# Performance work log

Hardware: AMD Instinct MI355X
Metric: run time of the kernel (lower is better)

## Reference

```python
import jax, jax.numpy as jnp
import numpy as np

B = 256        # batch of LLR frames
N = 576        # code length (from wman_N0576_R34_z24)
MR = 144       # check rows = N * (1 - 3/4)
Z = 24         # lifting factor
IT = 3         # decoding iterations
ROW_DEG = 15   # check-node degree (WiMAX rate-3/4)


def setup_inputs() -> dict:
    key = jax.random.key(0)
    r = jax.random.normal(key, (B, N), dtype=jnp.float32)
    # Deterministic sparse Tanner graph: 15 ones per check row (>=2 required for top-2)
    rng = np.random.RandomState(0)
    Hnp = np.zeros((MR, N), dtype=np.int32)
    cols = np.argsort(rng.rand(MR, N), axis=1)[:, :ROW_DEG]
    Hnp[np.arange(MR)[:, None], cols] = 1
    H = jnp.asarray(Hnp)
    alpha = jnp.ones((MR // Z, N // Z, IT), dtype=jnp.float32) * 0.7
    beta = jnp.ones((MR // Z, N // Z, IT), dtype=jnp.float32) * 0.05
    return {"r": r, "alpha": alpha, "beta": beta, "H": H}


def _decode(r, alpha, beta, Hf):
    # r: (B, N) channel LLRs; Hf: (MR, N) float 0/1 parity-check mask
    mask = Hf == 1.0
    node = jnp.arange(N)[None, None, :]           # (1, 1, N)
    M = Hf[None, :, :] * r[:, None, :]            # initial v->c messages (B, MR, N)
    E = jnp.zeros_like(M)
    n_it = alpha.shape[-1]
    for it in range(n_it):
        a = jnp.repeat(jnp.repeat(alpha[:, :, it], Z, axis=0), Z, axis=1)  # (MR, N)
        bt = jnp.repeat(jnp.repeat(beta[:, :, it], Z, axis=0), Z, axis=1)  # (MR, N)
        # check -> variable: masked min-2 magnitude + extrinsic sign product
        abs_M = jnp.abs(M)
        masked = jnp.where(mask, abs_M, jnp.inf)
        neg_vals, idx = jax.lax.top_k(-masked, 2)  # two smallest per check row
        min_vals = -neg_vals                        # (B, MR, 2)
        # exclude self: use 2nd min at the argmin position, 1st min elsewhere
        E_abs = jnp.where(node == idx[..., 0:1], min_vals[..., 1:2], min_vals[..., 0:1])
        signs = jnp.where(mask, jnp.sign(M), 1.0)
        row_sign_prod = jnp.prod(signs, axis=2, keepdims=True)
        E_sign = row_sign_prod * signs              # extrinsic sign
        E = a * E_sign * jax.nn.relu(E_abs - bt) * Hf
        # variable -> check: sum-minus-self
        sum_E = jnp.sum(E, axis=1, keepdims=True)   # (B, 1, N)
        M = (r[:, None, :] + sum_E - E) * Hf
    return r + jnp.sum(E, axis=1)                   # posterior LLRs (B, N)


def reference(r, alpha, beta, H):
    return _decode(r, alpha, beta, H.astype(jnp.float32))
```

## Files before the change

### kernel.cpp

```cpp
#include <hip/hip_runtime.h>

#define BATCH   256
#define NCOL    576
#define MROW    144
#define ZLIFT   24
#define NIT     3
#define ROW_DEG 15
#define NEDGE   (MROW * ROW_DEG)
#define NSCIT   ((MROW/ZLIFT) * (NCOL/ZLIFT) * NIT)
#define TPB     512

__global__ __launch_bounds__(256) void build_cols_kernel(
    const int* __restrict__ H, int* __restrict__ pk)
{
    const int wave = (blockIdx.x * blockDim.x + threadIdx.x) >> 6;
    const int lane = threadIdx.x & 63;
    if (wave >= MROW) return;
    const int* row = H + (size_t)wave * NCOL;
    const int srow = (wave / ZLIFT) * (NCOL / ZLIFT);
    int base = 0;
    #pragma unroll
    for (int c0 = 0; c0 < NCOL; c0 += 64) {
        const int n = c0 + lane;
        const int present = (row[n] != 0) ? 1 : 0;
        const unsigned long long mask = __ballot(present);
        if (present) {
            const int rank = __popcll(mask & ((1ull << lane) - 1ull));
            const int idx = base + rank;
            if (idx < ROW_DEG)
                pk[wave * ROW_DEG + idx] = n | ((srow + n / ZLIFT) << 16);
        }
        base += __popcll(mask);
    }
}

__global__ __launch_bounds__(TPB) void ldpc_decode_kernel(
    const float* __restrict__ r,
    const float* __restrict__ alpha,
    const float* __restrict__ beta,
    const int*   __restrict__ pk,
    float*       __restrict__ out)
{
    __shared__ float r_s[NCOL];
    __shared__ float cs[2][NCOL];
    __shared__ float E_s[NEDGE];
    __shared__ float a_s[NSCIT];
    __shared__ float b_s[NSCIT];
    __shared__ int   cdeg[NCOL];
    __shared__ int   cstart[NCOL];

    const int b   = blockIdx.x;
    const int tid = threadIdx.x;

    for (int n = tid; n < NCOL; n += TPB) {
        r_s[n]   = r[(size_t)b * NCOL + n];
        cs[0][n] = 0.0f;
        cdeg[n]  = 0;
    }
    if (tid < NSCIT) { a_s[tid] = alpha[tid]; b_s[tid] = beta[tid]; }
    __syncthreads();

    const bool is_row = (tid < MROW);
    int   pk_r[ROW_DEG];
    float r_r[ROW_DEG];
    float E_r[ROW_DEG];
    int   slot_r[ROW_DEG];
    if (is_row) {
        #pragma unroll
        for (int k = 0; k < ROW_DEG; ++k) {
            const int p = pk[tid * ROW_DEG + k];
            pk_r[k] = p;
            const int n = p & 0xFFFF;
            r_r[k]  = r_s[n];
            E_r[k]  = 0.0f;
            slot_r[k] = atomicAdd(&cdeg[n], 1);
        }
    }
    __syncthreads();

    if (tid < 64) {
        int local[9];
        int run = 0;
        #pragma unroll
        for (int j = 0; j < 9; ++j) { local[j] = cdeg[tid * 9 + j]; run += local[j]; }
        int scan = run;
        #pragma unroll
        for (int off = 1; off < 64; off <<= 1) {
            int up = __shfl_up(scan, off);
            if (tid >= off) scan += up;
        }
        int acc = scan - run;
        #pragma unroll
        for (int j = 0; j < 9; ++j) { cstart[tid * 9 + j] = acc; acc += local[j]; }
    }
    __syncthreads();

    if (is_row) {
        #pragma unroll
        for (int k = 0; k < ROW_DEG; ++k)
            slot_r[k] += cstart[pk_r[k] & 0xFFFF];
    }

    for (int it = 0; it < NIT; ++it) {
        float* prev = cs[it & 1];
        float* next = cs[(it + 1) & 1];

        if (is_row) {
            float vals[ROW_DEG];
            float min1 = INFINITY, min2 = INFINITY;
            int   kmin = -1;
            float sprod = 1.0f;
            #pragma unroll
            for (int k = 0; k < ROW_DEG; ++k) {
                const int n = pk_r[k] & 0xFFFF;
                const float v = r_r[k] + prev[n] - E_r[k];
                vals[k] = v;
                const float av = fabsf(v);
                const float s = (v > 0.0f) ? 1.0f : ((v < 0.0f) ? -1.0f : 0.0f);
                sprod *= s;
                if (av < min1)      { min2 = min1; min1 = av; kmin = k; }
                else if (av < min2) { min2 = av; }
            }
            #pragma unroll
            for (int k = 0; k < ROW_DEG; ++k) {
                const int sidx = pk_r[k] >> 16;
                const float v = vals[k];
                const float s = (v > 0.0f) ? 1.0f : ((v < 0.0f) ? -1.0f : 0.0f);
                const float a  = a_s[sidx * NIT + it];
                const float bt = b_s[sidx * NIT + it];
                const float eabs = (k == kmin) ? min2 : min1;
                float mag = eabs - bt;
                if (mag < 0.0f) mag = 0.0f;
                const float E = a * (sprod * s) * mag;
                E_r[k] = E;
                E_s[slot_r[k]] = E;
            }
        }
        __syncthreads();

        for (int n = tid; n < NCOL; n += TPB) {
            const int s0  = cstart[n];
            const int deg = cdeg[n];
            float sum = 0.0f;
            for (int i = 0; i < deg; ++i) sum += E_s[s0 + i];
            next[n] = sum;
        }
        __syncthreads();
    }

    const float* fin = cs[NIT & 1];
    for (int n = tid; n < NCOL; n += TPB)
        out[(size_t)b * NCOL + n] = r_s[n] + fin[n];
}

extern "C" void kernel_launch(void* const* d_in, const int* in_sizes, int n_in,
                              void* d_out, int out_size, void* d_ws, size_t ws_size,
                              hipStream_t stream) {
    const float* r     = (const float*)d_in[0];
    const float* alpha = (const float*)d_in[1];
    const float* beta  = (const float*)d_in[2];
    const int*   H     = (const int*)d_in[3];
    float* out = (float*)d_out;
    int*   pk  = (int*)d_ws;

    build_cols_kernel<<<(MROW * 64 + 255) / 256, 256, 0, stream>>>(H, pk);
    ldpc_decode_kernel<<<BATCH, TPB, 0, stream>>>(r, alpha, beta, pk, out);
}
```

Measured before the change: 72.78 us.

## Fuse parity-check column extraction into decode kernel and write output directly

Removes the separate kernel that compacts H into per-row column lists; each block now scans H itself with ballots and stores the list in shared memory. The last iteration writes posterior LLRs straight to global memory instead of going through a shared buffer and an extra barrier. This removes a launch and an inter-kernel dependency. In exchange, every block redundantly reads the whole H matrix, which adds L2 traffic and prologue latency.

Result: slower. 117.8 us (+61.8%).

```diff
diff --git a/kernel.cpp b/kernel.cpp
--- a/kernel.cpp
+++ b/kernel.cpp
@@ -9,36 +9,13 @@
 #define NEDGE   (MROW * ROW_DEG)
 #define NSCIT   ((MROW/ZLIFT) * (NCOL/ZLIFT) * NIT)
 #define TPB     512
+#define ROWS_PER_WAVE (MROW / 8)
 
-__global__ __launch_bounds__(256) void build_cols_kernel(
-    const int* __restrict__ H, int* __restrict__ pk)
-{
-    const int wave = (blockIdx.x * blockDim.x + threadIdx.x) >> 6;
-    const int lane = threadIdx.x & 63;
-    if (wave >= MROW) return;
-    const int* row = H + (size_t)wave * NCOL;
-    const int srow = (wave / ZLIFT) * (NCOL / ZLIFT);
-    int base = 0;
-    #pragma unroll
-    for (int c0 = 0; c0 < NCOL; c0 += 64) {
-        const int n = c0 + lane;
-        const int present = (row[n] != 0) ? 1 : 0;
-        const unsigned long long mask = __ballot(present);
-        if (present) {
-            const int rank = __popcll(mask & ((1ull << lane) - 1ull));
-            const int idx = base + rank;
-            if (idx < ROW_DEG)
-                pk[wave * ROW_DEG + idx] = n | ((srow + n / ZLIFT) << 16);
-        }
-        base += __popcll(mask);
-    }
-}
-
-__global__ __launch_bounds__(TPB) void ldpc_decode_kernel(
+__global__ __launch_bounds__(TPB) void ldpc_fused_kernel(
     const float* __restrict__ r,
     const float* __restrict__ alpha,
     const float* __restrict__ beta,
-    const int*   __restrict__ pk,
+    const int*   __restrict__ H,
     float*       __restrict__ out)
 {
     __shared__ float r_s[NCOL];
@@ -48,9 +25,12 @@
     __shared__ float b_s[NSCIT];
     __shared__ int   cdeg[NCOL];
     __shared__ int   cstart[NCOL];
+    __shared__ int   c_s[NEDGE];
 
-    const int b   = blockIdx.x;
-    const int tid = threadIdx.x;
+    const int b    = blockIdx.x;
+    const int tid  = threadIdx.x;
+    const int wave = tid >> 6;
+    const int lane = tid & 63;
 
     for (int n = tid; n < NCOL; n += TPB) {
         r_s[n]   = r[(size_t)b * NCOL + n];
@@ -58,6 +38,27 @@
         cdeg[n]  = 0;
     }
     if (tid < NSCIT) { a_s[tid] = alpha[tid]; b_s[tid] = beta[tid]; }
+
+    #pragma unroll
+    for (int j = 0; j < ROWS_PER_WAVE; ++j) {
+        const int row  = wave * ROWS_PER_WAVE + j;
+        const int srow = (row / ZLIFT) * (NCOL / ZLIFT);
+        const int* hrow = H + (size_t)row * NCOL;
+        int base = 0;
+        #pragma unroll
+        for (int c0 = 0; c0 < NCOL; c0 += 64) {
+            const int n = c0 + lane;
+            const int present = (hrow[n] != 0) ? 1 : 0;
+            const unsigned long long mask = __ballot(present);
+            if (present) {
+                const int rank = __popcll(mask & ((1ull << lane) - 1ull));
+                const int idx = base + rank;
+                if (idx < ROW_DEG)
+                    c_s[row * ROW_DEG + idx] = n | ((srow + n / ZLIFT) << 16);
+            }
+            base += __popcll(mask);
+        }
+    }
     __syncthreads();
 
     const bool is_row = (tid < MROW);
@@ -68,7 +69,7 @@
     if (is_row) {
         #pragma unroll
         for (int k = 0; k < ROW_DEG; ++k) {
-            const int p = pk[tid * ROW_DEG + k];
+            const int p = c_s[tid * ROW_DEG + k];
             pk_r[k] = p;
             const int n = p & 0xFFFF;
             r_r[k]  = r_s[n];
@@ -138,19 +139,25 @@
         }
         __syncthreads();
 
-        for (int n = tid; n < NCOL; n += TPB) {
-            const int s0  = cstart[n];
-            const int deg = cdeg[n];
-            float sum = 0.0f;
-            for (int i = 0; i < deg; ++i) sum += E_s[s0 + i];
-            next[n] = sum;
+        if (it < NIT - 1) {
+            for (int n = tid; n < NCOL; n += TPB) {
+                const int s0  = cstart[n];
+                const int deg = cdeg[n];
+                float sum = 0.0f;
+                for (int i = 0; i < deg; ++i) sum += E_s[s0 + i];
+                next[n] = sum;
+            }
+            __syncthreads();
+        } else {
+            for (int n = tid; n < NCOL; n += TPB) {
+                const int s0  = cstart[n];
+                const int deg = cdeg[n];
+                float sum = 0.0f;
+                for (int i = 0; i < deg; ++i) sum += E_s[s0 + i];
+                out[(size_t)b * NCOL + n] = r_s[n] + sum;
+            }
         }
-        __syncthreads();
     }
-
-    const float* fin = cs[NIT & 1];
-    for (int n = tid; n < NCOL; n += TPB)
-        out[(size_t)b * NCOL + n] = r_s[n] + fin[n];
 }
 
 extern "C" void kernel_launch(void* const* d_in, const int* in_sizes, int n_in,
@@ -161,8 +168,7 @@
     const float* beta  = (const float*)d_in[2];
     const int*   H     = (const int*)d_in[3];
     float* out = (float*)d_out;
-    int*   pk  = (int*)d_ws;
+    (void)d_ws; (void)ws_size;
 
-    build_cols_kernel<<<(MROW * 64 + 255) / 256, 256, 0, stream>>>(H, pk);
-    ldpc_decode_kernel<<<BATCH, TPB, 0, stream>>>(r, alpha, beta, pk, out);
+    ldpc_fused_kernel<<<BATCH, TPB, 0, stream>>>(r, alpha, beta, H, out);
 }
```
